# Optimization experiments

Hardware: AMD Instinct MI355X
Metric: run time of the kernel (lower is better)

## Reference

```python
import jax, jax.numpy as jnp
import numpy as np

K = 16
NUM_CLASSES = 1000
TAU = 0.2
LOGIT_SCALE = 20.0


def setup_inputs() -> dict:
    key = jax.random.key(0)
    k1, k2, k3, k4, k5 = jax.random.split(key, 5)
    B, D, N = 2048, 256, 100000
    x = jax.random.normal(k1, (B, D), dtype=jnp.float32)
    mean = jax.random.normal(k2, (D,), dtype=jnp.float32)
    std = jax.random.uniform(k3, (D,), dtype=jnp.float32, minval=0.5, maxval=1.5)
    mem_features = jax.random.normal(k4, (N, D), dtype=jnp.float32)
    mem_labels = jax.random.randint(k5, (N,), 0, NUM_CLASSES)
    return {"x": x, "mean": mean, "std": std,
            "mem_features": mem_features, "mem_labels": mem_labels}


def reference(x, mean, std, mem_features, mem_labels):
    # preprocess: standardize then L2-normalize rows (eval mode, no noise)
    x = (x - mean) / std
    norm = jnp.maximum(jnp.linalg.norm(x, axis=1, keepdims=True), 1e-6)
    x = x / norm
    # dense cosine similarity: [B, N]
    sims = jnp.einsum('bd,nd->bn', x, mem_features)
    # top-k neighbors per query
    top_sims, top_idx = jax.lax.top_k(sims, K)          # [B, K]
    top_lbl = mem_labels[top_idx]                       # [B, K]
    weights = jax.nn.softmax(top_sims / max(1e-6, TAU), axis=1)
    # scatter-add softmax weights into class logits
    B = x.shape[0]
    rows = jnp.arange(B)[:, None]                       # [B, 1]
    logits = jnp.zeros((B, NUM_CLASSES), dtype=x.dtype).at[rows, top_lbl].add(weights)
    return logits * LOGIT_SCALE
```

## Files before the change

### kernel.cpp

```cpp
#include <hip/hip_runtime.h>
#include <math.h>

constexpr int BQ   = 2048;
constexpr int D    = 256;
constexpr int NMEM = 100000;
constexpr int TOPK = 16;
constexpr int NCLS = 1000;
constexpr float TAU = 0.2f;
constexpr float LOGIT_SCALE = 20.0f;

constexpr int KTOT = 256;
constexpr int BK   = 64;
constexpr int TM   = 128;
constexpr int TN   = 128;
constexpr int CTILES = 13;
constexpr int CHUNK  = TN * CTILES;
constexpr int NCH    = 64;
constexpr int RBLK   = BQ / TM;
constexpr int NBLK   = RBLK * NCH;
constexpr int TOTAL_IT = CTILES * (KTOT / BK);
constexpr float XSCALE = 16.0f;
constexpr float INV_XS = 0.0625f;
constexpr float THR    = 3.0f;
constexpr float THRS   = 48.0f;
constexpr int CAP    = 512;
constexpr int MSEL   = 64;
constexpr int SELCAP = 96;
constexpr float NEG  = -3.0e38f;

using f32x4  = __attribute__((ext_vector_type(4))) float;

__device__ __forceinline__ unsigned f2e4m3(float f) {
    const unsigned u = __float_as_uint(f);
    const unsigned s = (u >> 24) & 0x80u;
    const int e = (int)((u >> 23) & 0xff);
    int te = e - 120;
    if (te <= 0) return s;
    const unsigned m = u & 0x7fffffu;
    const unsigned r = m + 0x7ffffu + ((m >> 20) & 1u);
    unsigned keep;
    if (r & 0x800000u) { ++te; keep = 0; } else keep = (r >> 20) & 7u;
    if (te >= 16 || (te == 15 && keep == 7)) return s | 0x7eu;
    return s | ((unsigned)te << 3) | keep;
}

__device__ __forceinline__ void load_lds16(const void* g, void* l) {
    __builtin_amdgcn_global_load_lds((const __attribute__((address_space(1))) void*)g,
                                     (__attribute__((address_space(3))) void*)l,
                                     16, 0, 0);
}

__global__ __launch_bounds__(256) void knn_prep(
    const float* __restrict__ x, const float* __restrict__ mean,
    const float* __restrict__ stdv, unsigned char* __restrict__ A1,
    float* __restrict__ XN, int* __restrict__ cnt)
{
    const int row = blockIdx.x;
    const int t = threadIdx.x;
    float v = (x[row * D + t] - mean[t]) / stdv[t];
    float s = v * v;
    #pragma unroll
    for (int off = 32; off > 0; off >>= 1) s += __shfl_down(s, off, 64);
    __shared__ float wsum[4];
    __shared__ float nrm;
    const int lane = t & 63, wid = t >> 6;
    if (lane == 0) wsum[wid] = s;
    __syncthreads();
    if (t == 0) {
        nrm = fmaxf(sqrtf(wsum[0] + wsum[1] + wsum[2] + wsum[3]), 1e-6f);
        cnt[row] = 0;
    }
    __syncthreads();
    const float xnv = v / nrm;
    A1[(size_t)row * KTOT + t] = (unsigned char)f2e4m3(xnv * XSCALE);
    XN[(size_t)row * D + t] = xnv;
}

__global__ __launch_bounds__(256) void knn_convb(
    const float* __restrict__ mem, unsigned char* __restrict__ B1)
{
    const int tid = threadIdx.x;
    const int rloc = tid >> 5, t = tid & 31;
    const long n = (long)blockIdx.x * 8 + rloc;
    if (n >= NMEM) return;
    const float* src = mem + n * D + t * 8;
    const float4 v0 = *(const float4*)(src);
    const float4 v1 = *(const float4*)(src + 4);
    const float f[8] = {v0.x, v0.y, v0.z, v0.w, v1.x, v1.y, v1.z, v1.w};
    unsigned long long pk = 0;
    #pragma unroll
    for (int i = 0; i < 8; ++i)
        pk |= (unsigned long long)f2e4m3(f[i]) << (8 * i);
    *(unsigned long long*)(B1 + n * KTOT + t * 8) = pk;
}

__global__ __launch_bounds__(256, 4) void knn_gemm_topk(
    const unsigned char* __restrict__ A1, const unsigned char* __restrict__ B1,
    int* __restrict__ cnt, uint2* __restrict__ cand_buf)
{
    __shared__ alignas(16) unsigned char As[2][TM * BK];
    __shared__ alignas(16) unsigned char Bs[2][TN * BK];

    const int tid  = threadIdx.x;
    const int lane = tid & 63, wave = tid >> 6;
    const int wm = wave >> 1, wn = wave & 1;
    const int lr  = lane & 15;
    const int q   = lane >> 4;
    const int lro = q * 4;

    const int nblk = blockIdx.x;
    const int xcd = nblk & 7, bi = nblk >> 3;
    const int rb = bi & 15;
    const int ch = (bi >> 4) + 8 * xcd;
    const int row0  = rb * TM;
    const int cbase = ch * CHUNK;

    int aoff[4][2], boff[4][2];
    #pragma unroll
    for (int i = 0; i < 4; ++i) {
        const int ra  = wm * 64 + i * 16 + lr;
        const int rbw = wn * 64 + i * 16 + lr;
        #pragma unroll
        for (int ks = 0; ks < 2; ++ks) {
            const int L = ks * 2 + (q >> 1);
            aoff[i][ks] = ra  * BK + (((L - (ra  >> 1)) & 3) << 4) + ((q & 1) << 3);
            boff[i][ks] = rbw * BK + (((L - (rbw >> 1)) & 3) << 4) + ((q & 1) << 3);
        }
    }

    const unsigned char* aSrc[2];
    int cSub[2], bSeg[2];
    #pragma unroll
    for (int s = 0; s < 2; ++s) {
        const int ci = s * 256 + tid;
        const int r = ci >> 2, sl = ci & 3;
        aSrc[s] = A1 + (size_t)(row0 + r) * KTOT + (((sl + (r >> 1)) & 3) << 4);
        cSub[s] = r;
        bSeg[s] = ((sl + (r >> 1)) & 3) << 4;
    }
    const unsigned char* bB[2];
    auto computeBB = [&](int tile) {
        #pragma unroll
        for (int s = 0; s < 2; ++s) {
            int candi = cbase + tile * TN + cSub[s];
            if (candi >= NMEM) candi = NMEM - 1;
            bB[s] = B1 + (size_t)candi * KTOT + bSeg[s];
        }
    };

    f32x4 acc[4][4];
    #pragma unroll
    for (int i = 0; i < 4; ++i)
        #pragma unroll
        for (int j = 0; j < 4; ++j)
            #pragma unroll
            for (int r = 0; r < 4; ++r) acc[i][j][r] = 0.f;

    int t = 0, kk = 0, p = 0;
    computeBB(0);
    {
        #pragma unroll
        for (int s = 0; s < 2; ++s)
            load_lds16(aSrc[s], (char*)As[0] + s * 4096 + wave * 1024);
        #pragma unroll
        for (int s = 0; s < 2; ++s)
            load_lds16(bB[s], (char*)Bs[0] + s * 4096 + wave * 1024);
    }
    __syncthreads();

    for (int it = 0; it < TOTAL_IT; ++it) {
        const bool last = (kk == KTOT - BK);
        const int tn = last ? t + 1 : t;
        const int kn = last ? 0 : kk + BK;

        const char* Ab = (const char*)As[p];
        const char* Bb = (const char*)Bs[p];
        long af[4][2], bf8[4][2];
        #pragma unroll
        for (int i = 0; i < 4; ++i)
            #pragma unroll
            for (int ks = 0; ks < 2; ++ks) {
                af[i][ks]  = *(const long*)(Ab + aoff[i][ks]);
                bf8[i][ks] = *(const long*)(Bb + boff[i][ks]);
            }

        if (tn < CTILES) {
            if (last) computeBB(tn);
            #pragma unroll
            for (int s = 0; s < 2; ++s)
                load_lds16(aSrc[s] + kn, (char*)As[p ^ 1] + s * 4096 + wave * 1024);
            #pragma unroll
            for (int s = 0; s < 2; ++s)
                load_lds16(bB[s] + kn, (char*)Bs[p ^ 1] + s * 4096 + wave * 1024);
        }

        #pragma unroll
        for (int ks = 0; ks < 2; ++ks)
            #pragma unroll
            for (int i = 0; i < 4; ++i)
                #pragma unroll
                for (int j = 0; j < 4; ++j)
                    acc[i][j] = __builtin_amdgcn_mfma_f32_16x16x32_fp8_fp8(
                        af[i][ks], bf8[j][ks], acc[i][j], 0, 0, 0);

        __syncthreads();

        if (last) {
            const int tb = cbase + t * TN;
            #pragma unroll
            for (int i = 0; i < 4; ++i) {
                const int rg = row0 + wm * 64 + i * 16 + lro;
                #pragma unroll
                for (int j = 0; j < 4; ++j) {
                    const int cidx = tb + wn * 64 + j * 16 + lr;
                    #pragma unroll
                    for (int r = 0; r < 4; ++r) {
                        const float v = acc[i][j][r];
                        if (v > THRS && cidx < NMEM) {
                            const int pos = atomicAdd(&cnt[rg + r], 1);
                            if (pos < CAP)
                                cand_buf[(size_t)(rg + r) * CAP + pos] =
                                    make_uint2(__float_as_uint(v * INV_XS),
                                               (unsigned)cidx);
                        }
                        acc[i][j][r] = 0.f;
                    }
                }
            }
        }
        t = tn; kk = kn; p ^= 1;
    }
}

__global__ __launch_bounds__(256) void knn_final(
    const int* __restrict__ cnt, const uint2* __restrict__ cand_buf,
    const float* __restrict__ xn, const float* __restrict__ mem,
    const int* __restrict__ labels, float* __restrict__ out)
{
    constexpr float BSCALE = 200.0f;
    __shared__ float cls[NCLS];
    __shared__ float xrow[D];
    __shared__ uint2 cl[CAP];
    __shared__ int   hist[1024];
    __shared__ int   psum[256];
    __shared__ float tstar;
    __shared__ int   scount;
    __shared__ int   seli[SELCAP];
    __shared__ float ex[SELCAP];
    __shared__ float fs[TOPK];
    __shared__ int   fi[TOPK];
    __shared__ float zshare;

    const int row = blockIdx.x;
    const int tid = threadIdx.x;
    const int lane = tid & 63, w = tid >> 6;

    for (int c = tid; c < NCLS; c += 256) cls[c] = 0.f;
    for (int i = tid; i < 1024; i += 256) hist[i] = 0;
    xrow[tid] = xn[(size_t)row * D + tid];
    int n = cnt[row]; if (n > CAP) n = CAP;
    for (int i = tid; i < n; i += 256) cl[i] = cand_buf[(size_t)row * CAP + i];
    if (tid == 0) scount = 0;
    __syncthreads();

    for (int i = tid; i < n; i += 256) {
        const float v = __uint_as_float(cl[i].x);
        int b = (int)((v - THR) * BSCALE);
        b = max(0, min(1023, b));
        atomicAdd(&hist[b], 1);
    }
    __syncthreads();
    psum[tid] = hist[4 * tid] + hist[4 * tid + 1] + hist[4 * tid + 2] + hist[4 * tid + 3];
    __syncthreads();
    if (tid == 0) {
        int cum = 0, g = 255;
        for (; g >= 0; --g) {
            if (cum + psum[g] >= MSEL) break;
            cum += psum[g];
        }
        float t = THR;
        if (g >= 0) {
            int bb = 4 * g + 3;
            for (; bb > 4 * g; --bb) {
                cum += hist[bb];
                if (cum >= MSEL) break;
            }
            if (bb == 4 * g) cum += hist[bb];
            t = THR + (float)bb * (1.0f / BSCALE);
        }
        tstar = t;
    }
    __syncthreads();
    for (int i = tid; i < n; i += 256) {
        const float v = __uint_as_float(cl[i].x);
        if (v >= tstar) {
            const int p = atomicAdd(&scount, 1);
            if (p < SELCAP) seli[p] = (int)cl[i].y;
        }
    }
    __syncthreads();
    int ns = scount; if (ns > SELCAP) ns = SELCAP;

    for (int c = w; c < ns; c += 4) {
        const float* m = mem + (size_t)seli[c] * D;
        float s = xrow[lane]       * m[lane]
                + xrow[lane + 64]  * m[lane + 64]
                + xrow[lane + 128] * m[lane + 128]
                + xrow[lane + 192] * m[lane + 192];
        #pragma unroll
        for (int off = 32; off > 0; off >>= 1) s += __shfl_down(s, off, 64);
        if (lane == 0) ex[c] = s;
    }
    __syncthreads();

    if (tid == 0) {
        float kmin = NEG; int kslot = 0;
        #pragma unroll
        for (int s = 0; s < TOPK; ++s) { fs[s] = NEG; fi[s] = -1; }
        for (int c = 0; c < ns; ++c) {
            const float v = ex[c];
            if (v > kmin) {
                fs[kslot] = v; fi[kslot] = seli[c];
                kmin = fs[0]; kslot = 0;
                #pragma unroll
                for (int s = 1; s < TOPK; ++s) {
                    const float tq = fs[s];
                    if (tq < kmin) { kmin = tq; kslot = s; }
                }
            }
        }
        float smax = fs[0];
        #pragma unroll
        for (int s = 1; s < TOPK; ++s) smax = fmaxf(smax, fs[s]);
        float e[TOPK]; float Z = 0.f;
        #pragma unroll
        for (int s = 0; s < TOPK; ++s) {
            e[s] = (fi[s] >= 0) ? expf((fs[s] - smax) * (1.0f / TAU)) : 0.f;
            Z += e[s];
        }
        for (int s = 0; s < TOPK; ++s) {
            if (fi[s] >= 0) cls[labels[fi[s]]] += e[s];
        }
        zshare = Z;
    }
    __syncthreads();
    const float scale = LOGIT_SCALE / zshare;
    for (int c = tid; c < NCLS; c += 256)
        out[(size_t)row * NCLS + c] = cls[c] * scale;
}

extern "C" void kernel_launch(void* const* d_in, const int* in_sizes, int n_in,
                              void* d_out, int out_size, void* d_ws, size_t ws_size,
                              hipStream_t stream) {
    (void)in_sizes; (void)n_in; (void)out_size; (void)ws_size;
    const float* x    = (const float*)d_in[0];
    const float* mean = (const float*)d_in[1];
    const float* stdv = (const float*)d_in[2];
    const float* mem  = (const float*)d_in[3];
    const int*   lbl  = (const int*)d_in[4];
    float* out = (float*)d_out;

    unsigned char* A1 = (unsigned char*)d_ws;
    float* XN = (float*)(A1 + (size_t)BQ * KTOT);
    unsigned char* B1 = (unsigned char*)(XN + (size_t)BQ * D);
    int* cnt = (int*)(B1 + (size_t)NMEM * KTOT);
    uint2* cand = (uint2*)(cnt + BQ);

    knn_prep<<<BQ, 256, 0, stream>>>(x, mean, stdv, A1, XN, cnt);
    knn_convb<<<(NMEM + 7) / 8, 256, 0, stream>>>(mem, B1);
    knn_gemm_topk<<<NBLK, 256, 0, stream>>>(A1, B1, cnt, cand);
    knn_final<<<BQ, 256, 0, stream>>>(cnt, cand, XN, mem, lbl, out);
}
```

Measured before the change: 374.8 us.

## Switch FP8 GEMM to 32x32x64 scaled MFMA and vectorize rescoring loads

Replaces the 16x16x32 fp8 MFMA tiling with the gfx950 32x32x64 f8f6f4 scaled MFMA, using unit scales. Each wave now issues four larger MFMAs per K-step instead of thirty-two small ones, with 128-bit LDS fragment loads and a remapped epilogue for the 32x32 accumulator layout. The final rescoring kernel also loads the query row and memory rows as float4 per lane, dropping the shared xrow buffer. The aim is higher matrix-core throughput and fewer instructions, at the cost of a more intricate register layout and possible LDS bank-conflict changes.

```diff
diff --git a/kernel.cpp b/kernel.cpp
--- a/kernel.cpp
+++ b/kernel.cpp
@@ -28,7 +28,9 @@
 constexpr int SELCAP = 96;
 constexpr float NEG  = -3.0e38f;
 
-using f32x4  = __attribute__((ext_vector_type(4))) float;
+using i32x4  = __attribute__((ext_vector_type(4))) int;
+using i32x8  = __attribute__((ext_vector_type(8))) int;
+using f32x16 = __attribute__((ext_vector_type(16))) float;
 
 __device__ __forceinline__ unsigned f2e4m3(float f) {
     const unsigned u = __float_as_uint(f);
@@ -104,9 +106,8 @@
     const int tid  = threadIdx.x;
     const int lane = tid & 63, wave = tid >> 6;
     const int wm = wave >> 1, wn = wave & 1;
-    const int lr  = lane & 15;
-    const int q   = lane >> 4;
-    const int lro = q * 4;
+    const int l31 = lane & 31;
+    const int kb  = lane >> 5;
 
     const int nblk = blockIdx.x;
     const int xcd = nblk & 7, bi = nblk >> 3;
@@ -115,16 +116,15 @@
     const int row0  = rb * TM;
     const int cbase = ch * CHUNK;
 
-    int aoff[4][2], boff[4][2];
-    #pragma unroll
-    for (int i = 0; i < 4; ++i) {
-        const int ra  = wm * 64 + i * 16 + lr;
-        const int rbw = wn * 64 + i * 16 + lr;
-        #pragma unroll
-        for (int ks = 0; ks < 2; ++ks) {
-            const int L = ks * 2 + (q >> 1);
-            aoff[i][ks] = ra  * BK + (((L - (ra  >> 1)) & 3) << 4) + ((q & 1) << 3);
-            boff[i][ks] = rbw * BK + (((L - (rbw >> 1)) & 3) << 4) + ((q & 1) << 3);
+    int aoff[2][2], boff[2][2];
+    #pragma unroll
+    for (int ti = 0; ti < 2; ++ti) {
+        const int ar = wm * 64 + ti * 32 + l31;
+        const int br = wn * 64 + ti * 32 + l31;
+        #pragma unroll
+        for (int c = 0; c < 2; ++c) {
+            aoff[ti][c] = ar * BK + (((2 * kb + c) - (ar >> 1)) & 3) * 16;
+            boff[ti][c] = br * BK + (((2 * kb + c) - (br >> 1)) & 3) * 16;
         }
     }
 
@@ -148,13 +148,13 @@
         }
     };
 
-    f32x4 acc[4][4];
-    #pragma unroll
-    for (int i = 0; i < 4; ++i)
-        #pragma unroll
-        for (int j = 0; j < 4; ++j)
-            #pragma unroll
-            for (int r = 0; r < 4; ++r) acc[i][j][r] = 0.f;
+    f32x16 acc[2][2];
+    #pragma unroll
+    for (int i = 0; i < 2; ++i)
+        #pragma unroll
+        for (int j = 0; j < 2; ++j)
+            #pragma unroll
+            for (int r = 0; r < 16; ++r) acc[i][j][r] = 0.f;
 
     int t = 0, kk = 0, p = 0;
     computeBB(0);
@@ -173,16 +173,18 @@
         const int tn = last ? t + 1 : t;
         const int kn = last ? 0 : kk + BK;
 
-        const char* Ab = (const char*)As[p];
-        const char* Bb = (const char*)Bs[p];
-        long af[4][2], bf8[4][2];
-        #pragma unroll
-        for (int i = 0; i < 4; ++i)
-            #pragma unroll
-            for (int ks = 0; ks < 2; ++ks) {
-                af[i][ks]  = *(const long*)(Ab + aoff[i][ks]);
-                bf8[i][ks] = *(const long*)(Bb + boff[i][ks]);
-            }
+        const unsigned char* Ab = As[p];
+        const unsigned char* Bb = Bs[p];
+        i32x8 Afr[2], Bfr[2];
+        #pragma unroll
+        for (int ti = 0; ti < 2; ++ti) {
+            const i32x4 alo = *(const i32x4*)(Ab + aoff[ti][0]);
+            const i32x4 ahi = *(const i32x4*)(Ab + aoff[ti][1]);
+            Afr[ti] = __builtin_shufflevector(alo, ahi, 0, 1, 2, 3, 4, 5, 6, 7);
+            const i32x4 blo = *(const i32x4*)(Bb + boff[ti][0]);
+            const i32x4 bhi = *(const i32x4*)(Bb + boff[ti][1]);
+            Bfr[ti] = __builtin_shufflevector(blo, bhi, 0, 1, 2, 3, 4, 5, 6, 7);
+        }
 
         if (tn < CTILES) {
             if (last) computeBB(tn);
@@ -195,35 +197,35 @@
         }
 
         #pragma unroll
-        for (int ks = 0; ks < 2; ++ks)
-            #pragma unroll
-            for (int i = 0; i < 4; ++i)
-                #pragma unroll
-                for (int j = 0; j < 4; ++j)
-                    acc[i][j] = __builtin_amdgcn_mfma_f32_16x16x32_fp8_fp8(
-                        af[i][ks], bf8[j][ks], acc[i][j], 0, 0, 0);
+        for (int ti = 0; ti < 2; ++ti)
+            #pragma unroll
+            for (int tj = 0; tj < 2; ++tj)
+                acc[ti][tj] = __builtin_amdgcn_mfma_scale_f32_32x32x64_f8f6f4(
+                    Afr[ti], Bfr[tj], acc[ti][tj], 0, 0,
+                    0, 0x7f7f7f7f, 0, 0x7f7f7f7f);
 
         __syncthreads();
 
         if (last) {
             const int tb = cbase + t * TN;
             #pragma unroll
-            for (int i = 0; i < 4; ++i) {
-                const int rg = row0 + wm * 64 + i * 16 + lro;
+            for (int ti = 0; ti < 2; ++ti) {
+                const int rb0 = row0 + wm * 64 + ti * 32 + 4 * kb;
                 #pragma unroll
-                for (int j = 0; j < 4; ++j) {
-                    const int cidx = tb + wn * 64 + j * 16 + lr;
+                for (int tj = 0; tj < 2; ++tj) {
+                    const int cidx = tb + wn * 64 + tj * 32 + l31;
                     #pragma unroll
-                    for (int r = 0; r < 4; ++r) {
-                        const float v = acc[i][j][r];
+                    for (int r = 0; r < 16; ++r) {
+                        const float v = acc[ti][tj][r];
                         if (v > THRS && cidx < NMEM) {
-                            const int pos = atomicAdd(&cnt[rg + r], 1);
+                            const int rg = rb0 + (r & 3) + 8 * (r >> 2);
+                            const int pos = atomicAdd(&cnt[rg], 1);
                             if (pos < CAP)
-                                cand_buf[(size_t)(rg + r) * CAP + pos] =
+                                cand_buf[(size_t)rg * CAP + pos] =
                                     make_uint2(__float_as_uint(v * INV_XS),
                                                (unsigned)cidx);
                         }
-                        acc[i][j][r] = 0.f;
+                        acc[ti][tj][r] = 0.f;
                     }
                 }
             }
@@ -239,7 +241,6 @@
 {
     constexpr float BSCALE = 200.0f;
     __shared__ float cls[NCLS];
-    __shared__ float xrow[D];
     __shared__ uint2 cl[CAP];
     __shared__ int   hist[1024];
     __shared__ int   psum[256];
@@ -255,9 +256,10 @@
     const int tid = threadIdx.x;
     const int lane = tid & 63, w = tid >> 6;
 
+    const float4 xr = *(const float4*)(xn + (size_t)row * D + lane * 4);
+
     for (int c = tid; c < NCLS; c += 256) cls[c] = 0.f;
     for (int i = tid; i < 1024; i += 256) hist[i] = 0;
-    xrow[tid] = xn[(size_t)row * D + tid];
     int n = cnt[row]; if (n > CAP) n = CAP;
     for (int i = tid; i < n; i += 256) cl[i] = cand_buf[(size_t)row * CAP + i];
     if (tid == 0) scount = 0;
@@ -302,11 +304,8 @@
     int ns = scount; if (ns > SELCAP) ns = SELCAP;
 
     for (int c = w; c < ns; c += 4) {
-        const float* m = mem + (size_t)seli[c] * D;
-        float s = xrow[lane]       * m[lane]
-                + xrow[lane + 64]  * m[lane + 64]
-                + xrow[lane + 128] * m[lane + 128]
-                + xrow[lane + 192] * m[lane + 192];
+        const float4 mv = *(const float4*)(mem + (size_t)seli[c] * D + lane * 4);
+        float s = xr.x * mv.x + xr.y * mv.y + xr.z * mv.z + xr.w * mv.w;
         #pragma unroll
         for (int off = 32; off > 0; off >>= 1) s += __shfl_down(s, off, 64);
         if (lane == 0) ex[c] = s;
```

Result: no change. 381.4 us (+1.8%).
